# Kernel tuning notes

Hardware: AMD Instinct MI355X
Metric: run time of the kernel (lower is better)

## Reference

```python
import jax, jax.numpy as jnp
import numpy as np

SELECT_SIZE = 64
SM_SCALE = 0.07216878364870322  # 192 ** -0.5
V_HEAD_DIM = 128


def setup_inputs() -> dict:
    key = jax.random.key(0)
    k1, k2, k3, k4 = jax.random.split(key, 4)
    B, S, Hq, G, TOPK = 4, 2048, 16, 4, 16
    T = B * S
    NB = S // SELECT_SIZE  # 32 blocks per sequence
    q = jax.random.normal(k1, (T, Hq, 192), dtype=jnp.float32)
    k = jax.random.normal(k2, (T, Hq, 192), dtype=jnp.float32)
    v = jax.random.normal(k3, (T, Hq, V_HEAD_DIM), dtype=jnp.float32)
    idx = jax.random.randint(k4, (T, G, TOPK), 0, NB, dtype=jnp.int32)
    # guarantee block 0 is always selected so every causal row has >=1 valid key
    idx = idx.at[..., 0].set(0)
    idx = jnp.sort(idx, axis=-1)
    return {"q": q, "k": k, "v": v, "selected_indices": idx,
            "batch_size": B, "seq_len": S}


def reference(q, k, v, selected_indices, batch_size, seq_len):
    B, S = batch_size, seq_len
    Hq = q.shape[1]
    G = selected_indices.shape[1]
    Hg = Hq // G  # query heads per selection-score group
    nb = (S + SELECT_SIZE - 1) // SELECT_SIZE
    dv = v.shape[-1]

    # un-ragged: B equal-length sequences
    qg = q.reshape(B, S, G, Hg, -1)
    kg = k.reshape(B, S, G, Hg, -1)
    vg = v.reshape(B, S, G, Hg, -1)
    idx = selected_indices.reshape(B, S, G, -1)

    # which KV blocks are selected for each (query position, group): [B,S,G,nb]
    allowed_blk = (idx[..., None] == jnp.arange(nb, dtype=idx.dtype)).any(axis=-2)
    blk_of_pos = jnp.arange(S) // SELECT_SIZE
    pos_ok = allowed_blk[..., blk_of_pos]  # [B, Tq, G, Skv]
    causal = jnp.arange(S)[:, None] >= jnp.arange(S)[None, :]
    mask = pos_ok & causal[None, :, None, :]          # [B, Tq, G, Skv]
    mask = mask.transpose(0, 2, 1, 3)[:, :, None]      # [B, G, 1, Tq, Skv]

    scores = jnp.einsum('btghd,bsghd->bghts', qg, kg) * SM_SCALE
    scores = jnp.where(mask, scores, jnp.float32(-1e30))
    attn = jax.nn.softmax(scores, axis=-1)
    o = jnp.einsum('bghts,bsghd->btghd', attn, vg)
    return o.reshape(B * S, Hq * dv)
```

## Files before the change

kernel.cpp:

```cpp
#include <hip/hip_runtime.h>


typedef __attribute__((ext_vector_type(8))) _Float16 half8;
typedef __attribute__((ext_vector_type(4))) float f32x4;
typedef __attribute__((ext_vector_type(4))) unsigned int u32x4;

__device__ __forceinline__ half8 cvt8(const float4* p) {
  float4 a = p[0], b = p[1];
  half8 r;
  r[0] = (_Float16)a.x; r[1] = (_Float16)a.y; r[2] = (_Float16)a.z; r[3] = (_Float16)a.w;
  r[4] = (_Float16)b.x; r[5] = (_Float16)b.y; r[6] = (_Float16)b.z; r[7] = (_Float16)b.w;
  return r;
}

__device__ __forceinline__ half8 cvt8s(const float4* p, float s) {
  float4 a = p[0], b = p[1];
  half8 r;
  r[0] = (_Float16)(a.x * s); r[1] = (_Float16)(a.y * s);
  r[2] = (_Float16)(a.z * s); r[3] = (_Float16)(a.w * s);
  r[4] = (_Float16)(b.x * s); r[5] = (_Float16)(b.y * s);
  r[6] = (_Float16)(b.z * s); r[7] = (_Float16)(b.w * s);
  return r;
}

__device__ __forceinline__ void async16(const void* g, void* l) {
  __builtin_amdgcn_global_load_lds(
      (const __attribute__((address_space(1))) void*)g,
      (__attribute__((address_space(3))) void*)l, 16, 0, 0);
}

__device__ __forceinline__ f32x4 vmax4(f32x4 a, f32x4 b) {
  f32x4 r;
  r[0] = fmaxf(a[0], b[0]); r[1] = fmaxf(a[1], b[1]);
  r[2] = fmaxf(a[2], b[2]); r[3] = fmaxf(a[3], b[3]);
  return r;
}

__global__ __launch_bounds__(256) void kv_prep(const float* __restrict__ k,
                                               const float* __restrict__ v,
                                               _Float16* __restrict__ kf,
                                               _Float16* __restrict__ vf) {
  __shared__ float lb[64 * 196];
  int blk = blockIdx.x;
  int bh = blk >> 5, kb = blk & 31;
  int b = bh >> 4, h = bh & 15;
  int tid = threadIdx.x;

  const float* ksrc = k + ((long)(b * 2048 + kb * 64) * 16 + h) * 192;
#pragma unroll
  for (int it = 0; it < 12; ++it) {
    int idx = it * 256 + tid;
    int kk = idx / 48, c4 = idx - kk * 48;
    *(float4*)(&lb[kk * 196 + c4 * 4]) = *(const float4*)(ksrc + (long)kk * 3072 + c4 * 4);
  }
  __syncthreads();
  _Float16* kdst = kf + (long)blk * 12288;
#pragma unroll
  for (int it = 0; it < 6; ++it) {
    int oct = it * 256 + tid;
    int frag = oct >> 6, lane = oct & 63;
    int ntile = frag / 6, kc = frag - ntile * 6;
    int lm = lane & 15;
    int n = ((lm >> 2) << 4) + ntile * 4 + (lm & 3);
    int d = kc * 32 + ((lane >> 4) << 3);
    *(half8*)(kdst + (long)oct * 8) = cvt8((const float4*)(&lb[n * 196 + d]));
  }
  __syncthreads();

  const float* vsrc = v + ((long)(b * 2048 + kb * 64) * 16 + h) * 128;
#pragma unroll
  for (int it = 0; it < 8; ++it) {
    int idx = it * 256 + tid;
    int kk = idx >> 5, c4 = idx & 31;
    *(float4*)(&lb[kk * 132 + c4 * 4]) = *(const float4*)(vsrc + (long)kk * 2048 + c4 * 4);
  }
  __syncthreads();
  _Float16* vdst = vf + (long)blk * 8192;
#pragma unroll
  for (int it = 0; it < 4; ++it) {
    int oct = it * 256 + tid;
    int frag = oct >> 6, lane = oct & 63;
    int n0 = frag >> 1, kc = frag & 1;
    int dv = n0 * 16 + (lane & 15);
    int kbase = kc * 32 + ((lane >> 4) << 3);
    half8 o;
#pragma unroll
    for (int j = 0; j < 8; ++j) o[j] = (_Float16)lb[(kbase + j) * 132 + dv];
    *(half8*)(vdst + (long)oct * 8) = o;
  }
}

__global__ __launch_bounds__(256) void attn_main(const float* __restrict__ q,
                                                 const int* __restrict__ idx,
                                                 const _Float16* __restrict__ kf,
                                                 const _Float16* __restrict__ vf,
                                                 float* __restrict__ out) {
  constexpr float SCL = 0.07216878364870322f * 1.4426950408889634f;
  int id = (int)blockIdx.x;
  int qb = 31 - (id >> 6);
  int h = id & 15, b = (id >> 4) & 3, g = h >> 2;
  int tid = threadIdx.x;
  int w = tid >> 6, L = tid & 63;
  int Lm = L & 15, Lq = L >> 4;
  int m0 = w * 16;
  int t0 = b * 2048 + qb * 64;

  __shared__ __align__(16) char sh_k[2][24576];
  __shared__ __align__(16) _Float16 Pbuf[4][16 * 72];
  __shared__ unsigned un_sh[4];

  const char* kfb = (const char*)(kf + (long)((b * 16 + h) * 32) * 12288);
  const _Float16* vfb = vf + (long)((b * 16 + h) * 32) * 8192;
  _Float16* pw = &Pbuf[w][0];

  auto stageK = [&](int kb, char* dst) {
    const char* kg = kfb + (long)kb * 24576;
#pragma unroll
    for (int c = 0; c < 6; ++c) {
      int ch = w + c * 4;
      async16(kg + ch * 1024 + L * 16, dst + ch * 1024);
    }
  };

  half8 vr[16];
  auto loadV = [&](int kb) {
    const half8* vg = (const half8*)(vfb + (long)kb * 8192);
#pragma unroll
    for (int j = 0; j < 16; ++j) vr[j] = vg[j * 64 + L];
  };

  half8 qa[6];
  const float* qrow = q + ((long)(t0 + m0 + Lm) * 16 + h) * 192;
#pragma unroll
  for (int c = 0; c < 6; ++c) qa[c] = cvt8s((const float4*)(qrow + c * 32 + Lq * 8), SCL);

  stageK(0, sh_k[0]);
  loadV(0);

  unsigned mrow;
  {
    const int4* ip = (const int4*)(idx + ((long)(t0 + m0 + Lm) * 4 + g) * 16);
    int4 iv = ip[Lq];
    unsigned mr = (1u << iv.x) | (1u << iv.y) | (1u << iv.z) | (1u << iv.w);
    mr |= __shfl_xor(mr, 16);
    mr |= __shfl_xor(mr, 32);
    mrow = mr;
  }
  unsigned un = mrow;
  un |= __shfl_xor(un, 1);
  un |= __shfl_xor(un, 2);
  un |= __shfl_xor(un, 4);
  un |= __shfl_xor(un, 8);
  if (L == 0) un_sh[w] = un;
  __syncthreads();
  unsigned bm = un_sh[0] | un_sh[1] | un_sh[2] | un_sh[3];
  unsigned bmask = bm & ((2u << qb) - 1);

  f32x4 Oacc[8];
#pragma unroll
  for (int n0 = 0; n0 < 8; ++n0) Oacc[n0] = (f32x4){0.f, 0.f, 0.f, 0.f};
  float m_i = -1e30f, l_i = 0.f;

  unsigned rem = bmask;
  int kb = 0;
  int cur = 0;

  for (;;) {
    rem &= rem - 1;
    int nxt = rem ? (int)__builtin_ctz(rem) : -1;
    if (nxt >= 0) stageK(nxt, sh_k[cur ^ 1]);

    const half8* lkf = (const half8*)sh_k[cur];

    f32x4 S[4];
#pragma unroll
    for (int nt = 0; nt < 4; ++nt) {
      f32x4 acc = {0.f, 0.f, 0.f, 0.f};
#pragma unroll
      for (int c = 0; c < 6; ++c)
        acc = __builtin_amdgcn_mfma_f32_16x16x32_f16(lkf[(nt * 6 + c) * 64 + L], qa[c], acc, 0, 0, 0);
      S[nt] = acc;
    }

    float p[4][4];
    float msel = ((mrow >> kb) & 1u) ? 1.0f : 0.0f;
    if (kb != qb) {
      f32x4 t = vmax4(vmax4(S[0], S[1]), vmax4(S[2], S[3]));
      float rmax = fmaxf(fmaxf(t[0], t[1]), fmaxf(t[2], t[3]));
      rmax = fmaxf(rmax, __shfl_xor(rmax, 16));
      rmax = fmaxf(rmax, __shfl_xor(rmax, 32));
      if (__any(rmax > m_i)) {
        float mn = fmaxf(m_i, rmax);
        float av = __builtin_amdgcn_exp2f(m_i - mn);
        m_i = mn;
        l_i *= av;
#pragma unroll
        for (int n0 = 0; n0 < 8; ++n0) Oacc[n0] *= av;
      }
      float ps[4];
#pragma unroll
      for (int nt = 0; nt < 4; ++nt) {
        float s0 = 0.f, s1 = 0.f;
#pragma unroll
        for (int i = 0; i < 4; i += 2) {
          float a = __builtin_amdgcn_exp2f(S[nt][i] - m_i) * msel;
          float c = __builtin_amdgcn_exp2f(S[nt][i + 1] - m_i) * msel;
          p[nt][i] = a; p[nt][i + 1] = c;
          s0 += a; s1 += c;
        }
        ps[nt] = s0 + s1;
      }
      float psum = (ps[0] + ps[1]) + (ps[2] + ps[3]);
      psum += __shfl_xor(psum, 16);
      psum += __shfl_xor(psum, 32);
      l_i += psum;
    } else {
      float sc[4][4];
      float rmax = -1e30f;
#pragma unroll
      for (int nt = 0; nt < 4; ++nt)
#pragma unroll
        for (int i = 0; i < 4; ++i) {
          int key = Lq * 16 + nt * 4 + i;
          bool ok = (msel != 0.f) && (key <= m0 + Lm);
          float v = ok ? S[nt][i] : -1e30f;
          sc[nt][i] = v;
          rmax = fmaxf(rmax, v);
        }
      rmax = fmaxf(rmax, __shfl_xor(rmax, 16));
      rmax = fmaxf(rmax, __shfl_xor(rmax, 32));
      float mn = fmaxf(m_i, rmax);
      float av = __builtin_amdgcn_exp2f(m_i - mn);
      m_i = mn;
      float ps[4];
#pragma unroll
      for (int nt = 0; nt < 4; ++nt) {
        float s0 = 0.f;
#pragma unroll
        for (int i = 0; i < 4; ++i) {
          float a = __builtin_amdgcn_exp2f(sc[nt][i] - mn);
          p[nt][i] = a;
          s0 += a;
        }
        ps[nt] = s0;
      }
      float psum = (ps[0] + ps[1]) + (ps[2] + ps[3]);
      psum += __shfl_xor(psum, 16);
      psum += __shfl_xor(psum, 32);
      l_i = l_i * av + psum;
#pragma unroll
      for (int n0 = 0; n0 < 8; ++n0) Oacc[n0] *= av;
    }

    asm volatile("s_waitcnt lgkmcnt(0)" ::: "memory");
    u32x4 w0, w1;
    {
      auto c00 = __builtin_amdgcn_cvt_pkrtz(p[0][0], p[0][1]);
      auto c01 = __builtin_amdgcn_cvt_pkrtz(p[0][2], p[0][3]);
      auto c10 = __builtin_amdgcn_cvt_pkrtz(p[1][0], p[1][1]);
      auto c11 = __builtin_amdgcn_cvt_pkrtz(p[1][2], p[1][3]);
      auto c20 = __builtin_amdgcn_cvt_pkrtz(p[2][0], p[2][1]);
      auto c21 = __builtin_amdgcn_cvt_pkrtz(p[2][2], p[2][3]);
      auto c30 = __builtin_amdgcn_cvt_pkrtz(p[3][0], p[3][1]);
      auto c31 = __builtin_amdgcn_cvt_pkrtz(p[3][2], p[3][3]);
      w0[0] = __builtin_bit_cast(unsigned, c00); w0[1] = __builtin_bit_cast(unsigned, c01);
      w0[2] = __builtin_bit_cast(unsigned, c10); w0[3] = __builtin_bit_cast(unsigned, c11);
      w1[0] = __builtin_bit_cast(unsigned, c20); w1[1] = __builtin_bit_cast(unsigned, c21);
      w1[2] = __builtin_bit_cast(unsigned, c30); w1[3] = __builtin_bit_cast(unsigned, c31);
    }
    *(u32x4*)(pw + Lm * 72 + Lq * 16) = w0;
    *(u32x4*)(pw + Lm * 72 + Lq * 16 + 8) = w1;
    asm volatile("s_waitcnt lgkmcnt(0)" ::: "memory");

#pragma unroll
    for (int kc = 0; kc < 2; ++kc) {
      half8 pfr = *(const half8*)(pw + Lm * 72 + kc * 32 + Lq * 8);
#pragma unroll
      for (int n0 = 0; n0 < 8; ++n0)
        Oacc[n0] = __builtin_amdgcn_mfma_f32_16x16x32_f16(vr[n0 * 2 + kc], pfr, Oacc[n0], 0, 0, 0);
    }

    if (nxt < 0) break;
    loadV(nxt);
    asm volatile("s_waitcnt vmcnt(16)\n\ts_barrier" ::: "memory");
    cur ^= 1;
    kb = nxt;
  }

  float inv = 1.f / l_i;
  float* orow = out + (long)(t0 + m0 + Lm) * 2048 + h * 128 + Lq * 4;
#pragma unroll
  for (int n0 = 0; n0 < 8; ++n0) {
    f32x4 o = Oacc[n0] * inv;
    *(f32x4*)(orow + n0 * 16) = o;
  }
}

extern "C" void kernel_launch(void* const* d_in, const int* in_sizes, int n_in,
                              void* d_out, int out_size, void* d_ws, size_t ws_size,
                              hipStream_t stream) {
  const float* q = (const float*)d_in[0];
  const float* k = (const float*)d_in[1];
  const float* v = (const float*)d_in[2];
  const int* idx = (const int*)d_in[3];
  _Float16* kf = (_Float16*)d_ws;
  _Float16* vf = kf + (size_t)2048 * 12288;
  float* out = (float*)d_out;
  kv_prep<<<2048, 256, 0, stream>>>(k, v, kf, vf);
  attn_main<<<2048, 256, 0, stream>>>(q, idx, kf, vf, out);
}
```

Before: 439.7 us.

## Stage V in LDS, single-buffer K, shuffle P fragments to raise occupancy

V tiles are no longer held in 16 registers per lane. They are now async-staged into shared memory alongside K, and the K double buffer is cut to a single buffer. The P matrix is passed between lanes with shuffles instead of an LDS round-trip, and the block mask is computed with one wave-wide shuffle reduction instead of a shared-memory barrier. Launch bounds request 4 blocks per CU to lower register and LDS pressure and raise occupancy. The cost is more barriers per iteration and less overlap between K/V loads and MFMA work.

```diff
diff --git a/kernel.cpp b/kernel.cpp
--- a/kernel.cpp
+++ b/kernel.cpp
@@ -90,11 +90,11 @@
   }
 }
 
-__global__ __launch_bounds__(256) void attn_main(const float* __restrict__ q,
-                                                 const int* __restrict__ idx,
-                                                 const _Float16* __restrict__ kf,
-                                                 const _Float16* __restrict__ vf,
-                                                 float* __restrict__ out) {
+__global__ __launch_bounds__(256, 4) void attn_main(const float* __restrict__ q,
+                                                    const int* __restrict__ idx,
+                                                    const _Float16* __restrict__ kf,
+                                                    const _Float16* __restrict__ vf,
+                                                    float* __restrict__ out) {
   constexpr float SCL = 0.07216878364870322f * 1.4426950408889634f;
   int id = (int)blockIdx.x;
   int qb = 31 - (id >> 6);
@@ -105,28 +105,25 @@
   int m0 = w * 16;
   int t0 = b * 2048 + qb * 64;
 
-  __shared__ __align__(16) char sh_k[2][24576];
-  __shared__ __align__(16) _Float16 Pbuf[4][16 * 72];
-  __shared__ unsigned un_sh[4];
+  __shared__ __align__(16) char sh_k[24576];
+  __shared__ __align__(16) char sh_v[16384];
 
   const char* kfb = (const char*)(kf + (long)((b * 16 + h) * 32) * 12288);
-  const _Float16* vfb = vf + (long)((b * 16 + h) * 32) * 8192;
-  _Float16* pw = &Pbuf[w][0];
-
-  auto stageK = [&](int kb, char* dst) {
-    const char* kg = kfb + (long)kb * 24576;
+  const char* vfb = (const char*)(vf + (long)((b * 16 + h) * 32) * 8192);
+
+  auto stageK = [&](int kb) {
 #pragma unroll
     for (int c = 0; c < 6; ++c) {
       int ch = w + c * 4;
-      async16(kg + ch * 1024 + L * 16, dst + ch * 1024);
+      async16(kfb + (long)kb * 24576 + ch * 1024 + L * 16, sh_k + ch * 1024);
     }
   };
-
-  half8 vr[16];
-  auto loadV = [&](int kb) {
-    const half8* vg = (const half8*)(vfb + (long)kb * 8192);
-#pragma unroll
-    for (int j = 0; j < 16; ++j) vr[j] = vg[j * 64 + L];
+  auto stageV = [&](int kb) {
+#pragma unroll
+    for (int c = 0; c < 4; ++c) {
+      int ch = w + c * 4;
+      async16(vfb + (long)kb * 16384 + ch * 1024 + L * 16, sh_v + ch * 1024);
+    }
   };
 
   half8 qa[6];
@@ -134,27 +131,22 @@
 #pragma unroll
   for (int c = 0; c < 6; ++c) qa[c] = cvt8s((const float4*)(qrow + c * 32 + Lq * 8), SCL);
 
-  stageK(0, sh_k[0]);
-  loadV(0);
-
-  unsigned mrow;
+  unsigned rm = 0;
   {
-    const int4* ip = (const int4*)(idx + ((long)(t0 + m0 + Lm) * 4 + g) * 16);
-    int4 iv = ip[Lq];
-    unsigned mr = (1u << iv.x) | (1u << iv.y) | (1u << iv.z) | (1u << iv.w);
-    mr |= __shfl_xor(mr, 16);
-    mr |= __shfl_xor(mr, 32);
-    mrow = mr;
-  }
-  unsigned un = mrow;
-  un |= __shfl_xor(un, 1);
-  un |= __shfl_xor(un, 2);
-  un |= __shfl_xor(un, 4);
-  un |= __shfl_xor(un, 8);
-  if (L == 0) un_sh[w] = un;
-  __syncthreads();
-  unsigned bm = un_sh[0] | un_sh[1] | un_sh[2] | un_sh[3];
+    const int4* ip = (const int4*)(idx + ((long)(t0 + L) * 4 + g) * 16);
+#pragma unroll
+    for (int u = 0; u < 4; ++u) {
+      int4 iv = ip[u];
+      rm |= (1u << iv.x) | (1u << iv.y) | (1u << iv.z) | (1u << iv.w);
+    }
+  }
+  unsigned bm = rm;
+#pragma unroll
+  for (int o = 1; o < 64; o <<= 1) bm |= __shfl_xor(bm, o, 64);
+  unsigned mrow = __shfl(rm, m0 + Lm, 64);
   unsigned bmask = bm & ((2u << qb) - 1);
+
+  stageK(0); stageV(0);
 
   f32x4 Oacc[8];
 #pragma unroll
@@ -163,15 +155,14 @@
 
   unsigned rem = bmask;
   int kb = 0;
-  int cur = 0;
 
   for (;;) {
     rem &= rem - 1;
     int nxt = rem ? (int)__builtin_ctz(rem) : -1;
-    if (nxt >= 0) stageK(nxt, sh_k[cur ^ 1]);
-
-    const half8* lkf = (const half8*)sh_k[cur];
-
+
+    asm volatile("s_waitcnt vmcnt(4)\n\ts_barrier" ::: "memory");
+
+    const half8* lkf = (const half8*)sh_k;
     f32x4 S[4];
 #pragma unroll
     for (int nt = 0; nt < 4; ++nt) {
@@ -181,6 +172,9 @@
         acc = __builtin_amdgcn_mfma_f32_16x16x32_f16(lkf[(nt * 6 + c) * 64 + L], qa[c], acc, 0, 0, 0);
       S[nt] = acc;
     }
+
+    asm volatile("s_waitcnt vmcnt(0) lgkmcnt(0)\n\ts_barrier" ::: "memory");
+    if (nxt >= 0) stageK(nxt);
 
     float p[4][4];
     float msel = ((mrow >> kb) & 1u) ? 1.0f : 0.0f;
@@ -252,38 +246,36 @@
       for (int n0 = 0; n0 < 8; ++n0) Oacc[n0] *= av;
     }
 
-    asm volatile("s_waitcnt lgkmcnt(0)" ::: "memory");
-    u32x4 w0, w1;
-    {
-      auto c00 = __builtin_amdgcn_cvt_pkrtz(p[0][0], p[0][1]);
-      auto c01 = __builtin_amdgcn_cvt_pkrtz(p[0][2], p[0][3]);
-      auto c10 = __builtin_amdgcn_cvt_pkrtz(p[1][0], p[1][1]);
-      auto c11 = __builtin_amdgcn_cvt_pkrtz(p[1][2], p[1][3]);
-      auto c20 = __builtin_amdgcn_cvt_pkrtz(p[2][0], p[2][1]);
-      auto c21 = __builtin_amdgcn_cvt_pkrtz(p[2][2], p[2][3]);
-      auto c30 = __builtin_amdgcn_cvt_pkrtz(p[3][0], p[3][1]);
-      auto c31 = __builtin_amdgcn_cvt_pkrtz(p[3][2], p[3][3]);
-      w0[0] = __builtin_bit_cast(unsigned, c00); w0[1] = __builtin_bit_cast(unsigned, c01);
-      w0[2] = __builtin_bit_cast(unsigned, c10); w0[3] = __builtin_bit_cast(unsigned, c11);
-      w1[0] = __builtin_bit_cast(unsigned, c20); w1[1] = __builtin_bit_cast(unsigned, c21);
-      w1[2] = __builtin_bit_cast(unsigned, c30); w1[3] = __builtin_bit_cast(unsigned, c31);
-    }
-    *(u32x4*)(pw + Lm * 72 + Lq * 16) = w0;
-    *(u32x4*)(pw + Lm * 72 + Lq * 16 + 8) = w1;
-    asm volatile("s_waitcnt lgkmcnt(0)" ::: "memory");
-
+    unsigned w8[8];
+#pragma unroll
+    for (int nt = 0; nt < 4; ++nt) {
+      w8[2 * nt]     = __builtin_bit_cast(unsigned, __builtin_amdgcn_cvt_pkrtz(p[nt][0], p[nt][1]));
+      w8[2 * nt + 1] = __builtin_bit_cast(unsigned, __builtin_amdgcn_cvt_pkrtz(p[nt][2], p[nt][3]));
+    }
+    half8 pfr[2];
 #pragma unroll
     for (int kc = 0; kc < 2; ++kc) {
-      half8 pfr = *(const half8*)(pw + Lm * 72 + kc * 32 + Lq * 8);
+      int src = ((Lq >> 1) + 2 * kc) * 16 + Lm;
+      u32x4 d;
+#pragma unroll
+      for (int u = 0; u < 4; ++u) {
+        unsigned lo = (unsigned)__shfl((int)w8[u], src, 64);
+        unsigned hi = (unsigned)__shfl((int)w8[u + 4], src, 64);
+        d[u] = (Lq & 1) ? hi : lo;
+      }
+      pfr[kc] = __builtin_bit_cast(half8, d);
+    }
+
+    const half8* lvf = (const half8*)sh_v;
+#pragma unroll
+    for (int kc = 0; kc < 2; ++kc)
 #pragma unroll
       for (int n0 = 0; n0 < 8; ++n0)
-        Oacc[n0] = __builtin_amdgcn_mfma_f32_16x16x32_f16(vr[n0 * 2 + kc], pfr, Oacc[n0], 0, 0, 0);
-    }
+        Oacc[n0] = __builtin_amdgcn_mfma_f32_16x16x32_f16(lvf[(n0 * 2 + kc) * 64 + L], pfr[kc], Oacc[n0], 0, 0, 0);
 
     if (nxt < 0) break;
-    loadV(nxt);
-    asm volatile("s_waitcnt vmcnt(16)\n\ts_barrier" ::: "memory");
-    cur ^= 1;
+    asm volatile("s_waitcnt lgkmcnt(0)\n\ts_barrier" ::: "memory");
+    stageV(nxt);
     kb = nxt;
   }
 
```

Result: faster. 414.9 us (-5.6%).
